# Performance work log

Hardware: AMD Instinct MI355X
Metric: run time of the kernel (lower is better)

Reference implementation:

```python
import jax, jax.numpy as jnp
import numpy as np

EPSILON = 0.05
MAX_ITER = 50
ALPHA = 6.0
THRESHOLD = 0.25
SCALE = 0.02  # keeps OT costs near THRESHOLD so the gate is not saturated


def setup_inputs() -> dict:
    key = jax.random.key(0)
    k1, k2 = jax.random.split(key)
    B, E, D, P = 8192, 8, 512, 32
    tokens = jax.random.normal(k1, (B, E, D), dtype=jnp.float32) * SCALE
    prototypes = jax.random.normal(k2, (E, P, D), dtype=jnp.float32) * SCALE
    return {"tokens": tokens, "prototypes": prototypes, "full_index": 0}


def _sinkhorn_log(cost, epsilon, max_iter):
    # cost: [..., n_source, n_target]; batched log-domain Sinkhorn, fixed iterations
    ns, nt = cost.shape[-2], cost.shape[-1]
    log_mu = jnp.full(cost.shape[:-1], -float(np.log(ns)), dtype=cost.dtype)
    log_nu = jnp.full(cost.shape[:-2] + (nt,), -float(np.log(nt)), dtype=cost.dtype)
    log_k = -cost / epsilon

    def step(carry, _):
        log_u, log_v = carry
        log_u = log_mu - jax.scipy.special.logsumexp(log_k + log_v[..., None, :], axis=-1)
        log_v = log_nu - jax.scipy.special.logsumexp(log_k + log_u[..., :, None], axis=-2)
        return (log_u, log_v), None

    (log_u, log_v), _ = jax.lax.scan(
        step, (jnp.zeros_like(log_mu), jnp.zeros_like(log_nu)), None, length=max_iter
    )
    return jnp.exp(log_k + log_u[..., :, None] + log_v[..., None, :])


def reference(tokens, prototypes, full_index):
    # tokens: [B, E, D], prototypes: [E, P, D]
    B, E, D = tokens.shape
    anchor = tokens[:, full_index, :]                                   # [B, D]
    source = jnp.stack(
        [tokens, jnp.broadcast_to(anchor[:, None, :], tokens.shape)], axis=2
    )                                                                   # [B, E, 2, D]
    # squared euclidean cdist: ||s||^2 - 2 s.p + ||p||^2
    s2 = jnp.sum(source * source, axis=-1)                              # [B, E, 2]
    p2 = jnp.sum(prototypes * prototypes, axis=-1)                      # [E, P]
    cross = jnp.einsum('besd,epd->besp', source, prototypes)            # [B, E, 2, P]
    cost = jnp.maximum(s2[..., None] - 2.0 * cross + p2[None, :, None, :], 0.0)
    transport = _sinkhorn_log(cost, EPSILON, MAX_ITER)                  # [B, E, 2, P]
    ot_cost = jnp.sum(transport * cost, axis=(-1, -2))                  # [B, E]
    validity = jax.nn.sigmoid(-ALPHA * (ot_cost - THRESHOLD))[..., None]  # [B, E, 1]
    # the full_index expert always passes with validity 1 and zero cost
    is_full = jnp.arange(E) == full_index                               # [E]
    ot_cost = jnp.where(is_full[None, :], 0.0, ot_cost)
    validity = jnp.where(is_full[None, :, None], 1.0, validity)
    return validity, ot_cost
```

## Files before the change

kernel.cpp:

```cpp
#include <hip/hip_runtime.h>
#include <hip/hip_bf16.h>


#define EXP2F(x) __builtin_amdgcn_exp2f(x)
#define LOG2F(x) __builtin_amdgcn_logf(x)
#define RCPF(x)  __builtin_amdgcn_rcpf(x)

typedef __bf16 bf16x8 __attribute__((ext_vector_type(8)));
typedef float  f32x4  __attribute__((ext_vector_type(4)));

#define BDIM 8192
#define EDIM 8
#define DDIM 512
#define PDIM 32
#define BPB  32
#define NTHR 256
#define PFD  4
#define C_SCALE 28.853900817779268f
#define LOG2E   1.4426950408889634f

template<int CTRL>
__device__ __forceinline__ float dpp_mov(float x) {
  return __int_as_float(__builtin_amdgcn_update_dpp(
      0, __float_as_int(x), CTRL, 0xF, 0xF, true));
}
__device__ __forceinline__ float dpp_sum8(float x) {
  x += dpp_mov<0xB1>(x);
  x += dpp_mov<0x4E>(x);
  x += dpp_mov<0x141>(x);
  return x;
}
__device__ __forceinline__ float dpp_max8(float x) {
  x = fmaxf(x, dpp_mov<0xB1>(x));
  x = fmaxf(x, dpp_mov<0x4E>(x));
  x = fmaxf(x, dpp_mov<0x141>(x));
  return x;
}

__device__ __forceinline__ bf16x8 cvt2(float4 a, float4 b) {
  bf16x8 r;
  r[0] = (__bf16)a.x; r[1] = (__bf16)a.y; r[2] = (__bf16)a.z; r[3] = (__bf16)a.w;
  r[4] = (__bf16)b.x; r[5] = (__bf16)b.y; r[6] = (__bf16)b.z; r[7] = (__bf16)b.w;
  return r;
}

__global__ __launch_bounds__(NTHR, 3)
void ot_noise_gate_kernel(const float* __restrict__ tokens,
                          const float* __restrict__ protos,
                          const int*   __restrict__ fullIndexPtr,
                          float*       __restrict__ out) {
  const int fi    = fullIndexPtr[0];
  const int e     = blockIdx.x & (EDIM - 1);
  const int b0    = (blockIdx.x >> 3) * BPB;
  float* outVal = out;
  float* outOt  = out + BDIM * EDIM;

  if (e == fi) {
    int t = threadIdx.x;
    if (t < BPB) {
      int b = b0 + t;
      outVal[b * EDIM + e] = 1.0f;
      outOt [b * EDIM + e] = 0.0f;
    }
    return;
  }

  __shared__ __align__(16) __bf16 sB[64 * PDIM * 8];
  __shared__ float sPNp[8][PDIM];
  __shared__ __align__(16) float sCw[4][16][36];

  const int t  = threadIdx.x;
  const int l  = t & 63;
  const int w  = t >> 6;
  const int fr = l & 15;
  const int q4 = l >> 4;

  const int bRow = b0 + 8 * w + (fr & 7);
  const int eSel = (fr < 8) ? e : fi;
  const float4* rp4 = (const float4*)(tokens + ((size_t)bRow * EDIM + eSel) * DDIM);

  float4 buf[PFD][2];
  #pragma unroll
  for (int c = 0; c < PFD; ++c) {
    buf[c][0] = rp4[c * 8 + q4 * 2];
    buf[c][1] = rp4[c * 8 + q4 * 2 + 1];
  }

  {
    const float4* pG4 = (const float4*)(protos + (size_t)e * PDIM * DDIM);
    const int p  = t & 31;
    const int oh = t >> 5;
    float pnp = 0.f;
    #pragma unroll
    for (int pass = 0; pass < 8; ++pass) {
      int oct = oh * 8 + pass;
      float4 a = pG4[p * 128 + oct * 2];
      float4 b = pG4[p * 128 + oct * 2 + 1];
      pnp += a.x*a.x + a.y*a.y + a.z*a.z + a.w*a.w
           + b.x*b.x + b.y*b.y + b.z*b.z + b.w*b.w;
      *(bf16x8*)&sB[(oct * PDIM + p) * 8] = cvt2(a, b);
    }
    sPNp[oh][p] = pnp;
  }
  __syncthreads();

  f32x4 acc0 = (f32x4){0.f, 0.f, 0.f, 0.f};
  f32x4 acc1 = (f32x4){0.f, 0.f, 0.f, 0.f};
  float ss = 0.f;

  #pragma unroll
  for (int kc = 0; kc < 16; ++kc) {
    float4 ca0 = buf[kc % PFD][0];
    float4 ca1 = buf[kc % PFD][1];
    if (kc < 16 - PFD) {
      buf[kc % PFD][0] = rp4[(kc + PFD) * 8 + q4 * 2];
      buf[kc % PFD][1] = rp4[(kc + PFD) * 8 + q4 * 2 + 1];
    }
    ss += ca0.x*ca0.x + ca0.y*ca0.y + ca0.z*ca0.z + ca0.w*ca0.w
        + ca1.x*ca1.x + ca1.y*ca1.y + ca1.z*ca1.z + ca1.w*ca1.w;
    bf16x8 aF  = cvt2(ca0, ca1);
    bf16x8 bF0 = *(const bf16x8*)&sB[((kc * 4 + q4) * PDIM + fr) * 8];
    bf16x8 bF1 = *(const bf16x8*)&sB[((kc * 4 + q4) * PDIM + 16 + fr) * 8];
    acc0 = __builtin_amdgcn_mfma_f32_16x16x32_bf16(aF, bF0, acc0, 0, 0, 0);
    acc1 = __builtin_amdgcn_mfma_f32_16x16x32_bf16(aF, bF1, acc1, 0, 0, 0);
  }

  ss += __shfl_xor(ss, 16);
  ss += __shfl_xor(ss, 32);
  float pn_a = 0.f, pn_b = 0.f;
  #pragma unroll
  for (int o = 0; o < 8; ++o) {
    pn_a += sPNp[o][fr];
    pn_b += sPNp[o][16 + fr];
  }

  #pragma unroll
  for (int reg = 0; reg < 4; ++reg) {
    int row = q4 * 4 + reg;
    float nrm = __shfl(ss, row);
    sCw[w][row][fr]      = fmaxf(nrm - 2.f * acc0[reg] + pn_a, 0.f);
    sCw[w][row][16 + fr] = fmaxf(nrm - 2.f * acc1[reg] + pn_b, 0.f);
  }

  const int i = l >> 3;
  const int s = l & 7;
  float c0[4], c1[4];
  {
    float4 v0 = *(const float4*)&sCw[w][i][4 * s];
    float4 v1 = *(const float4*)&sCw[w][8 + i][4 * s];
    c0[0] = v0.x; c0[1] = v0.y; c0[2] = v0.z; c0[3] = v0.w;
    c1[0] = v1.x; c1[1] = v1.y; c1[2] = v1.z; c1[3] = v1.w;
  }

  float W[4], dc[4];
  float sum0 = 0.f, mA = -1e30f, mB = -1e30f;
  #pragma unroll
  for (int r = 0; r < 4; ++r) {
    float ka = -c0[r] * C_SCALE, kb = -c1[r] * C_SCALE;
    dc[r] = c1[r] - c0[r];
    sum0 += c0[r];
    mA = fmaxf(mA, ka);
    mB = fmaxf(mB, kb);
  }
  mA = dpp_max8(mA);
  mB = dpp_max8(mB);
  float sa = 0.f, sb = 0.f;
  #pragma unroll
  for (int r = 0; r < 4; ++r) {
    float ka = -c0[r] * C_SCALE, kb = -c1[r] * C_SCALE;
    sa += EXP2F(ka - mA);
    sb += EXP2F(kb - mB);
    W[r] = EXP2F(C_SCALE * dc[r]);
  }
  sa   = dpp_sum8(sa);
  sb   = dpp_sum8(sb);
  sum0 = dpp_sum8(sum0);
  float delta = (mB + LOG2F(sb)) - (mA + LOG2F(sa));

  float updPrev = delta;
  float rPrev   = -1.f;
  bool  live    = true;
  for (int it = 0; it < 49; ++it) {
    float s2 = EXP2F(delta);
    float T = 0.f;
    #pragma unroll
    for (int r = 0; r < 4; ++r)
      T += RCPF(__builtin_fmaf(W[r], s2, 1.0f));
    T = dpp_sum8(T);
    float upd = LOG2F(T) - LOG2F(32.0f - T);
    float rr  = upd * RCPF(updPrev);
    bool small = fabsf(upd) <= 5e-7f;
    bool geo = live && !small && (it >= 3)
             && (rr > 0.001f) && (rr < 0.998f)
             && (fabsf(rr - rPrev) < 0.002f);
    float mrem = (float)(48 - it);
    float jump = geo
        ? upd * rr * (1.0f - EXP2F(mrem * LOG2F(rr))) * RCPF(1.0f - rr)
        : 0.0f;
    if (live) delta += upd + jump;
    live = live && !small && !geo;
    rPrev = rr; updPrev = upd;
    if (__ballot(live) == 0ull) break;
  }

  float s2 = EXP2F(delta), sv = 0.f;
  #pragma unroll
  for (int r = 0; r < 4; ++r)
    sv += RCPF(__builtin_fmaf(W[r], s2, 1.0f)) * dc[r];
  sv = dpp_sum8(sv);
  if (s == 0) {
    int b = b0 + 8 * w + i;
    float ot  = (sum0 + sv) * 0.03125f;
    float val = RCPF(1.0f + EXP2F(LOG2E * 6.0f * (ot - 0.25f)));
    outVal[b * EDIM + e] = val;
    outOt [b * EDIM + e] = ot;
  }
}

extern "C" void kernel_launch(void* const* d_in, const int* in_sizes, int n_in,
                              void* d_out, int out_size, void* d_ws, size_t ws_size,
                              hipStream_t stream) {
  const float* tokens = (const float*)d_in[0];
  const float* protos = (const float*)d_in[1];
  const int*   fidx   = (const int*)d_in[2];
  float* out = (float*)d_out;

  dim3 grid((BDIM / BPB) * EDIM);
  ot_noise_gate_kernel<<<grid, NTHR, 0, stream>>>(tokens, protos, fidx, out);
}
```

Before: 206.0 us.

## Precompute bf16 prototypes and norms in a prep kernel, DMA them to LDS

Adds a small prep kernel that converts the prototypes to bf16 once, in the swizzled LDS layout, and computes their squared norms into workspace. The main kernel then copies the bf16 tile straight into shared memory with global_load_lds and reads the norms directly. Previously every block reloaded and converted the fp32 prototypes and reduced the norms itself. The token prefetch depth also rises from 4 to 6, which costs extra registers and may affect occupancy at 3 blocks per CU. The change also adds a second kernel launch.

Measured after the change: 196.5 us. 4.6% less time.

```diff
diff --git a/kernel.cpp b/kernel.cpp
--- a/kernel.cpp
+++ b/kernel.cpp
@@ -15,9 +15,17 @@
 #define PDIM 32
 #define BPB  32
 #define NTHR 256
-#define PFD  4
+#define PFD  6
 #define C_SCALE 28.853900817779268f
 #define LOG2E   1.4426950408889634f
+
+#define GLOBAL_AS __attribute__((address_space(1)))
+#define LDS_AS    __attribute__((address_space(3)))
+
+__device__ __forceinline__ void gload_lds16(const void* g, void* l) {
+  __builtin_amdgcn_global_load_lds((GLOBAL_AS const void*)g,
+                                   (LDS_AS void*)l, 16, 0, 0);
+}
 
 template<int CTRL>
 __device__ __forceinline__ float dpp_mov(float x) {
@@ -44,9 +52,29 @@
   return r;
 }
 
+__global__ __launch_bounds__(256)
+void prep_protos_kernel(const float* __restrict__ protos,
+                        __bf16* __restrict__ pbf,
+                        float*  __restrict__ pnorm) {
+  const int idx = blockIdx.x * 256 + threadIdx.x;
+  const int oct = idx & 63;
+  const int ep  = idx >> 6;
+  const int p   = ep & 31;
+  const int e   = ep >> 5;
+  const float4* src = (const float4*)(protos + (size_t)ep * DDIM) + oct * 2;
+  float4 a = src[0], b = src[1];
+  float pnp = a.x*a.x + a.y*a.y + a.z*a.z + a.w*a.w
+            + b.x*b.x + b.y*b.y + b.z*b.z + b.w*b.w;
+  *(bf16x8*)&pbf[((size_t)e * 2048 + oct * 32 + p) * 8] = cvt2(a, b);
+  #pragma unroll
+  for (int d = 1; d < 64; d <<= 1) pnp += __shfl_xor(pnp, d);
+  if (oct == 0) pnorm[ep] = pnp;
+}
+
 __global__ __launch_bounds__(NTHR, 3)
 void ot_noise_gate_kernel(const float* __restrict__ tokens,
-                          const float* __restrict__ protos,
+                          const __bf16* __restrict__ pbf,
+                          const float*  __restrict__ pnorm,
                           const int*   __restrict__ fullIndexPtr,
                           float*       __restrict__ out) {
   const int fi    = fullIndexPtr[0];
@@ -66,7 +94,6 @@
   }
 
   __shared__ __align__(16) __bf16 sB[64 * PDIM * 8];
-  __shared__ float sPNp[8][PDIM];
   __shared__ __align__(16) float sCw[4][16][36];
 
   const int t  = threadIdx.x;
@@ -87,21 +114,15 @@
   }
 
   {
-    const float4* pG4 = (const float4*)(protos + (size_t)e * PDIM * DDIM);
-    const int p  = t & 31;
-    const int oh = t >> 5;
-    float pnp = 0.f;
+    const __bf16* pbfE = pbf + (size_t)e * 2048 * 8;
     #pragma unroll
-    for (int pass = 0; pass < 8; ++pass) {
-      int oct = oh * 8 + pass;
-      float4 a = pG4[p * 128 + oct * 2];
-      float4 b = pG4[p * 128 + oct * 2 + 1];
-      pnp += a.x*a.x + a.y*a.y + a.z*a.z + a.w*a.w
-           + b.x*b.x + b.y*b.y + b.z*b.z + b.w*b.w;
-      *(bf16x8*)&sB[(oct * PDIM + p) * 8] = cvt2(a, b);
+    for (int j = 0; j < 8; ++j) {
+      int f0 = w * 512 + j * 64;
+      gload_lds16(pbfE + (size_t)(f0 + l) * 8, &sB[(size_t)f0 * 8]);
     }
-    sPNp[oh][p] = pnp;
-  }
+  }
+  float pn_a = pnorm[e * PDIM + fr];
+  float pn_b = pnorm[e * PDIM + 16 + fr];
   __syncthreads();
 
   f32x4 acc0 = (f32x4){0.f, 0.f, 0.f, 0.f};
@@ -127,12 +148,6 @@
 
   ss += __shfl_xor(ss, 16);
   ss += __shfl_xor(ss, 32);
-  float pn_a = 0.f, pn_b = 0.f;
-  #pragma unroll
-  for (int o = 0; o < 8; ++o) {
-    pn_a += sPNp[o][fr];
-    pn_b += sPNp[o][16 + fr];
-  }
 
   #pragma unroll
   for (int reg = 0; reg < 4; ++reg) {
@@ -225,6 +240,10 @@
   const int*   fidx   = (const int*)d_in[2];
   float* out = (float*)d_out;
 
+  __bf16* pbf   = (__bf16*)d_ws;
+  float*  pnorm = (float*)((char*)d_ws + 256 * 1024);
+
+  prep_protos_kernel<<<64, 256, 0, stream>>>(protos, pbf, pnorm);
   dim3 grid((BDIM / BPB) * EDIM);
-  ot_noise_gate_kernel<<<grid, NTHR, 0, stream>>>(tokens, protos, fidx, out);
-}
+  ot_noise_gate_kernel<<<grid, NTHR, 0, stream>>>(tokens, pbf, pnorm, fidx, out);
+}
```
